# Kernel tuning notes

Measured on AMD Instinct MI355X. Metric: run time of the kernel, lower is better.

## Reference

```python
import jax, jax.numpy as jnp
import numpy as np

NEG_SLOPE = 0.2  # PyG GATConv default leaky_relu slope


def setup_inputs() -> dict:
    key = jax.random.key(0)
    ks = jax.random.split(key, 5)
    N, E, IN, OUT = 100000, 3200000, 256, 128
    x = jax.random.normal(ks[0], (N, IN), dtype=jnp.float32)
    edge_index = jax.random.randint(ks[1], (2, E), 0, N, dtype=jnp.int64)
    W = jax.random.normal(ks[2], (IN, OUT), dtype=jnp.float32) / np.sqrt(IN)
    att_src = jax.random.normal(ks[3], (OUT,), dtype=jnp.float32) / np.sqrt(OUT)
    att_dst = jax.random.normal(ks[4], (OUT,), dtype=jnp.float32) / np.sqrt(OUT)
    bias = jnp.zeros((OUT,), dtype=jnp.float32)
    return {"x": x, "edge_index": edge_index, "W": W, "att_src": att_src,
            "att_dst": att_dst, "bias": bias, "item_len": 1024}


def reference(x, edge_index, W, att_src, att_dst, bias, item_len):
    N = x.shape[0]
    # Linear projection (GATConv.lin), eval mode so dropouts are identity
    h = x @ W  # [N, OUT]
    # add self loops (PyG default add_self_loops=True)
    loop = jnp.arange(N, dtype=edge_index.dtype)
    src = jnp.concatenate([edge_index[0], loop])  # message sources j
    dst = jnp.concatenate([edge_index[1], loop])  # message targets i
    # per-node attention logits, then per-edge gather
    a_s = h @ att_src  # [N]
    a_d = h @ att_dst  # [N]
    e = jax.nn.leaky_relu(a_s[src] + a_d[dst], NEG_SLOPE)  # [E+N]
    # segment softmax over incoming edges of each target node
    m = jax.lax.stop_gradient(jax.ops.segment_max(e, dst, num_segments=N))
    p = jnp.exp(e - m[dst])
    z = jax.ops.segment_sum(p, dst, num_segments=N)  # >0 thanks to self loops
    alpha = p / z[dst]  # [E+N]
    # scatter-aggregate weighted messages
    out = jax.ops.segment_sum(alpha[:, None] * h[src], dst, num_segments=N) + bias
    xo = jax.nn.elu(out)  # F.elu after conv1
    # y = elu(sum(x[0] * x[1:item_len], dim=1))
    y = jax.nn.elu(jnp.sum(xo[0] * xo[1:item_len], axis=1))
    return y
```

## Files before the change

### kernel.cpp

```cpp
#include <hip/hip_runtime.h>
#include <hip/hip_bf16.h>

#define IN_DIM   256
#define OUT_DIM  128
#define KEEP     1024
#define CAP      128
#define NEG_SLOPE 0.2f

enum : size_t {
    WS_WS   = 0,
    WS_WD   = WS_WS + IN_DIM,
    WS_CUR  = WS_WD + IN_DIM,
    WS_BKT  = WS_CUR + KEEP,
    WS_XO   = WS_BKT + (size_t)KEEP*CAP,
    WS_END  = WS_XO + (size_t)KEEP*OUT_DIM
};

__device__ __forceinline__ float dot4(float4 a, float4 b) {
    return a.x*b.x + a.y*b.y + a.z*b.z + a.w*b.w;
}

__global__ void k0_fold(const float* __restrict__ W,
                        const float* __restrict__ att_src,
                        const float* __restrict__ att_dst,
                        float* __restrict__ ws, int* __restrict__ cur) {
    int c = threadIdx.x;
    const float* row = W + (size_t)c * OUT_DIM;
    float s = 0.f, d = 0.f;
    for (int o = 0; o < OUT_DIM; ++o) {
        float w = row[o];
        s += w * att_src[o];
        d += w * att_dst[o];
    }
    ws[WS_WS + c] = s;
    ws[WS_WD + c] = d;
    cur[c] = 0; cur[c + 256] = 0; cur[c + 512] = 0; cur[c + 768] = 0;
}

__global__ void kf_fill(const int* __restrict__ src, const int* __restrict__ dst,
                        int E, int* __restrict__ cur, int* __restrict__ bkt) {
    int stride = gridDim.x * blockDim.x;
    for (int e = blockIdx.x * blockDim.x + threadIdx.x; e < E; e += stride) {
        int d = dst[e];
        if ((unsigned)d < KEEP) {
            int p = atomicAdd(&cur[d], 1);
            if (p < CAP) bkt[d * CAP + p] = src[e];
        }
    }
}

__global__ void __launch_bounds__(256)
k5_agg(const float* __restrict__ x, const float* __restrict__ W,
       const float* __restrict__ bias, const float* __restrict__ ws,
       const int* __restrict__ cur, const int* __restrict__ bkt,
       float* __restrict__ xo) {
    __shared__ int   s_src[CAP];
    __shared__ float s_e[CAP];
    __shared__ float s_alpha[CAP];
    __shared__ float agg[IN_DIM];
    __shared__ float red[4];
    __shared__ float sh_self[2];
    __shared__ float sh_m, sh_z;
    __shared__ float proj[256];

    int i = blockIdx.x;
    int t = threadIdx.x;
    int wid = t >> 6, lane = t & 63;
    int cnt = min(cur[i], CAP);

    if (t < cnt) s_src[t] = bkt[i * CAP + t];
    __syncthreads();

    const float4* wsv = (const float4*)(ws + WS_WS);
    const float4* wdv = (const float4*)(ws + WS_WD);
    float4 wsl = wsv[lane];

    if (wid == 0) {
        float4 wdl = wdv[lane];
        const float4* xr = (const float4*)(x + (size_t)i * IN_DIM);
        float4 xv = xr[lane];
        float s = dot4(xv, wsl), d = dot4(xv, wdl);
        for (int o = 32; o; o >>= 1) { s += __shfl_down(s, o); d += __shfl_down(d, o); }
        if (lane == 0) { sh_self[0] = s; sh_self[1] = d; }
    }
    for (int k = wid; k < cnt; k += 4) {
        const float4* xr = (const float4*)(x + (size_t)s_src[k] * IN_DIM);
        float4 xv = xr[lane];
        float s = dot4(xv, wsl);
        for (int o = 32; o; o >>= 1) s += __shfl_down(s, o);
        if (lane == 0) s_e[k] = s;
    }
    __syncthreads();

    float ad_i = sh_self[1];
    float e_self = sh_self[0] + ad_i;
    e_self = e_self > 0.f ? e_self : NEG_SLOPE * e_self;
    if (t < cnt) {
        float v = s_e[t] + ad_i;
        s_e[t] = v > 0.f ? v : NEG_SLOPE * v;
    }
    __syncthreads();

    float m = e_self;
    for (int k = t; k < cnt; k += 256) m = fmaxf(m, s_e[k]);
    for (int o = 32; o; o >>= 1) m = fmaxf(m, __shfl_down(m, o));
    if (lane == 0) red[wid] = m;
    __syncthreads();
    if (t == 0) sh_m = fmaxf(fmaxf(red[0], red[1]), fmaxf(red[2], red[3]));
    __syncthreads();
    m = sh_m;

    float z = (t == 0) ? __expf(e_self - m) : 0.f;
    for (int k = t; k < cnt; k += 256) z += __expf(s_e[k] - m);
    for (int o = 32; o; o >>= 1) z += __shfl_down(z, o);
    if (lane == 0) red[wid] = z;
    __syncthreads();
    if (t == 0) sh_z = red[0] + red[1] + red[2] + red[3];
    __syncthreads();
    float inv_z = 1.f / sh_z;

    if (t < cnt) s_alpha[t] = __expf(s_e[t] - m) * inv_z;
    __syncthreads();

    float val = __expf(e_self - m) * inv_z * x[(size_t)i * IN_DIM + t];
    for (int k = 0; k < cnt; ++k)
        val += s_alpha[k] * x[(size_t)s_src[k] * IN_DIM + t];
    agg[t] = val;
    __syncthreads();

    int o = t & 127, half = t >> 7;
    float acc = 0.f;
    const float* wcol = W + o;
    int c0 = half * 128;
    for (int c = c0; c < c0 + 128; ++c) acc += agg[c] * wcol[(size_t)c * OUT_DIM];
    proj[t] = acc;
    __syncthreads();
    if (t < 128) {
        float outv = proj[t] + proj[t + 128] + bias[t];
        float xov = outv > 0.f ? outv : __expf(outv) - 1.f;
        xo[(size_t)i * OUT_DIM + t] = xov;
    }
}

__global__ void k6_final(const float* __restrict__ xo, float* __restrict__ y) {
    int k = blockIdx.x + 1;
    int t = threadIdx.x;
    float v = xo[t] * xo[(size_t)k * OUT_DIM + t];
    for (int o = 32; o; o >>= 1) v += __shfl_down(v, o);
    __shared__ float red[2];
    if ((t & 63) == 0) red[t >> 6] = v;
    __syncthreads();
    if (t == 0) {
        float s = red[0] + red[1];
        y[k - 1] = s > 0.f ? s : __expf(s) - 1.f;
    }
}

extern "C" void kernel_launch(void* const* d_in, const int* in_sizes, int n_in,
                              void* d_out, int out_size, void* d_ws, size_t ws_size,
                              hipStream_t stream) {
    const float* x       = (const float*)d_in[0];
    const int*   ei      = (const int*)d_in[1];
    const float* W       = (const float*)d_in[2];
    const float* att_src = (const float*)d_in[3];
    const float* att_dst = (const float*)d_in[4];
    const float* bias    = (const float*)d_in[5];

    int E = in_sizes[1] / 2;
    const int* src = ei;
    const int* dst = ei + E;

    float* ws  = (float*)d_ws;
    int*   wsi = (int*)d_ws;

    k0_fold<<<1, 256, 0, stream>>>(W, att_src, att_dst, ws, wsi + WS_CUR);
    kf_fill<<<2048, 256, 0, stream>>>(src, dst, E, wsi + WS_CUR, wsi + WS_BKT);
    k5_agg<<<KEEP, 256, 0, stream>>>(x, W, bias, ws, wsi + WS_CUR,
                                     wsi + WS_BKT, ws + WS_XO);
    k6_final<<<KEEP - 1, 128, 0, stream>>>(ws + WS_XO, (float*)d_out);
}
```

Baseline: 214.7 us.

## Cache neighbor rows in LDS, vectorize dst scan and attention fold

Each node's first 32 neighbor feature rows and its own row are kept in shared memory during the logit pass, so the aggregation loop reads them from LDS instead of fetching them from global memory a second time. The edge-fill kernel reads destination indices as int4 and runs on half as many blocks, and the weight/attention fold uses float4 loads. The added 32KB of shared memory per block may limit occupancy despite the launch-bounds hint.

```diff
diff --git a/kernel.cpp b/kernel.cpp
--- a/kernel.cpp
+++ b/kernel.cpp
@@ -5,6 +5,7 @@
 #define OUT_DIM  128
 #define KEEP     1024
 #define CAP      128
+#define LCAP     32
 #define NEG_SLOPE 0.2f
 
 enum : size_t {
@@ -25,12 +26,15 @@
                         const float* __restrict__ att_dst,
                         float* __restrict__ ws, int* __restrict__ cur) {
     int c = threadIdx.x;
-    const float* row = W + (size_t)c * OUT_DIM;
+    const float4* row = (const float4*)(W + (size_t)c * OUT_DIM);
+    const float4* asv = (const float4*)att_src;
+    const float4* adv = (const float4*)att_dst;
     float s = 0.f, d = 0.f;
-    for (int o = 0; o < OUT_DIM; ++o) {
-        float w = row[o];
-        s += w * att_src[o];
-        d += w * att_dst[o];
+    #pragma unroll 8
+    for (int o4 = 0; o4 < OUT_DIM / 4; ++o4) {
+        float4 w = row[o4];
+        s += dot4(w, asv[o4]);
+        d += dot4(w, adv[o4]);
     }
     ws[WS_WS + c] = s;
     ws[WS_WD + c] = d;
@@ -40,26 +44,36 @@
 __global__ void kf_fill(const int* __restrict__ src, const int* __restrict__ dst,
                         int E, int* __restrict__ cur, int* __restrict__ bkt) {
     int stride = gridDim.x * blockDim.x;
-    for (int e = blockIdx.x * blockDim.x + threadIdx.x; e < E; e += stride) {
+    int tid = blockIdx.x * blockDim.x + threadIdx.x;
+    const int4* dst4 = (const int4*)dst;
+    int E4 = E >> 2;
+    for (int e4 = tid; e4 < E4; e4 += stride) {
+        int4 d4 = dst4[e4];
+        int base = e4 << 2;
+        if ((unsigned)d4.x < KEEP) { int p = atomicAdd(&cur[d4.x], 1); if (p < CAP) bkt[d4.x * CAP + p] = src[base];     }
+        if ((unsigned)d4.y < KEEP) { int p = atomicAdd(&cur[d4.y], 1); if (p < CAP) bkt[d4.y * CAP + p] = src[base + 1]; }
+        if ((unsigned)d4.z < KEEP) { int p = atomicAdd(&cur[d4.z], 1); if (p < CAP) bkt[d4.z * CAP + p] = src[base + 2]; }
+        if ((unsigned)d4.w < KEEP) { int p = atomicAdd(&cur[d4.w], 1); if (p < CAP) bkt[d4.w * CAP + p] = src[base + 3]; }
+    }
+    for (int e = (E4 << 2) + tid; e < E; e += stride) {
         int d = dst[e];
-        if ((unsigned)d < KEEP) {
-            int p = atomicAdd(&cur[d], 1);
-            if (p < CAP) bkt[d * CAP + p] = src[e];
-        }
-    }
-}
-
-__global__ void __launch_bounds__(256)
+        if ((unsigned)d < KEEP) { int p = atomicAdd(&cur[d], 1); if (p < CAP) bkt[d * CAP + p] = src[e]; }
+    }
+}
+
+__global__ void __launch_bounds__(256, 4)
 k5_agg(const float* __restrict__ x, const float* __restrict__ W,
        const float* __restrict__ bias, const float* __restrict__ ws,
        const int* __restrict__ cur, const int* __restrict__ bkt,
        float* __restrict__ xo) {
+    __shared__ float s_rows[LCAP][IN_DIM];
+    __shared__ float s_self[IN_DIM];
     __shared__ int   s_src[CAP];
     __shared__ float s_e[CAP];
     __shared__ float s_alpha[CAP];
     __shared__ float agg[IN_DIM];
     __shared__ float red[4];
-    __shared__ float sh_self[2];
+    __shared__ float sh_sd[2];
     __shared__ float sh_m, sh_z;
     __shared__ float proj[256];
 
@@ -79,21 +93,23 @@
         float4 wdl = wdv[lane];
         const float4* xr = (const float4*)(x + (size_t)i * IN_DIM);
         float4 xv = xr[lane];
+        ((float4*)s_self)[lane] = xv;
         float s = dot4(xv, wsl), d = dot4(xv, wdl);
         for (int o = 32; o; o >>= 1) { s += __shfl_down(s, o); d += __shfl_down(d, o); }
-        if (lane == 0) { sh_self[0] = s; sh_self[1] = d; }
+        if (lane == 0) { sh_sd[0] = s; sh_sd[1] = d; }
     }
     for (int k = wid; k < cnt; k += 4) {
         const float4* xr = (const float4*)(x + (size_t)s_src[k] * IN_DIM);
         float4 xv = xr[lane];
+        if (k < LCAP) ((float4*)(s_rows[k]))[lane] = xv;
         float s = dot4(xv, wsl);
         for (int o = 32; o; o >>= 1) s += __shfl_down(s, o);
         if (lane == 0) s_e[k] = s;
     }
     __syncthreads();
 
-    float ad_i = sh_self[1];
-    float e_self = sh_self[0] + ad_i;
+    float ad_i = sh_sd[1];
+    float e_self = sh_sd[0] + ad_i;
     e_self = e_self > 0.f ? e_self : NEG_SLOPE * e_self;
     if (t < cnt) {
         float v = s_e[t] + ad_i;
@@ -122,8 +138,11 @@
     if (t < cnt) s_alpha[t] = __expf(s_e[t] - m) * inv_z;
     __syncthreads();
 
-    float val = __expf(e_self - m) * inv_z * x[(size_t)i * IN_DIM + t];
-    for (int k = 0; k < cnt; ++k)
+    float val = __expf(e_self - m) * inv_z * s_self[t];
+    int c1 = cnt < LCAP ? cnt : LCAP;
+    for (int k = 0; k < c1; ++k)
+        val += s_alpha[k] * s_rows[k][t];
+    for (int k = LCAP; k < cnt; ++k)
         val += s_alpha[k] * x[(size_t)s_src[k] * IN_DIM + t];
     agg[t] = val;
     __syncthreads();
@@ -174,7 +193,7 @@
     int*   wsi = (int*)d_ws;
 
     k0_fold<<<1, 256, 0, stream>>>(W, att_src, att_dst, ws, wsi + WS_CUR);
-    kf_fill<<<2048, 256, 0, stream>>>(src, dst, E, wsi + WS_CUR, wsi + WS_BKT);
+    kf_fill<<<1024, 256, 0, stream>>>(src, dst, E, wsi + WS_CUR, wsi + WS_BKT);
     k5_agg<<<KEEP, 256, 0, stream>>>(x, W, bias, ws, wsi + WS_CUR,
                                      wsi + WS_BKT, ws + WS_XO);
     k6_final<<<KEEP - 1, 128, 0, stream>>>(ws + WS_XO, (float*)d_out);
```

After: 213.1 us. Within noise of the previous version (-0.8%).
